# Optimization experiments

Measured on AMD Instinct MI355X. Metric: run time of the kernel, lower is better.

The kernel has to match this reference:

```python
import jax, jax.numpy as jnp
import numpy as np

OFFSET = (0, 0)
STRIDE = (2, 2)

B, C, H, W = 2, 256, 384, 384
N_ACTIVE = 16384
GRID = 192  # strided index grid: OFFSET + (GRID-1)*STRIDE < H


def setup_inputs() -> dict:
    key = jax.random.key(0)
    k1, k2, k3 = jax.random.split(key, 3)
    x = jax.random.normal(k1, (B, C, N_ACTIVE), dtype=jnp.float32)
    original_output = jax.random.normal(k2, (B, C, H, W), dtype=jnp.float32)
    active_indices = jax.random.randint(k3, (N_ACTIVE, 2), 0, GRID, dtype=jnp.int32)
    return {"x": x, "original_output": original_output, "active_indices": active_indices}


def reference(x, original_output, active_indices):
    # Scatter-write active values into the dense output at strided/offset coords.
    # write location for active index k: (OFFSET[0] + iy*STRIDE[0], OFFSET[1] + ix*STRIDE[1])
    h = OFFSET[0] + active_indices[:, 0] * STRIDE[0]  # [N]
    w = OFFSET[1] + active_indices[:, 1] * STRIDE[1]  # [N]
    # advanced indexing on the two spatial dims -> [B, C, N] slots, overwritten by x
    out = original_output.at[:, :, h, w].set(x)
    return out
```

## Files before the change

### kernel.cpp

```cpp
#include <hip/hip_runtime.h>

#define BB      2
#define CC      256
#define HH      384
#define WW      384
#define N_ACT   16384
#define GRID_N  192
#define NCELL   (GRID_N * GRID_N)
#define PLANE_F4 ((HH * WW) / 4)
#define ROW_F4   (WW / 4)
#define PAIRS_PER_PLANE (PLANE_F4 / 2)
#define BLK_PER_PLANE (PAIRS_PER_PLANE / 256)
#define NXCD    8

typedef float fx4 __attribute__((ext_vector_type(4)));

__global__ void winner_scatter_kernel(const int2* __restrict__ idx,
                                      int* __restrict__ winner) {
    int k = blockIdx.x * blockDim.x + threadIdx.x;
    if (k < N_ACT) {
        int2 p = idx[k];
        atomicMax(&winner[p.x * GRID_N + p.y], k);
    }
}

__global__ void scatter_main_kernel(const fx4* __restrict__ orig,
                                    const float* __restrict__ x,
                                    const int* __restrict__ winner,
                                    fx4* __restrict__ out) {
    int L   = blockIdx.x;
    int xcd = L & (NXCD - 1);
    int g   = L >> 3;
    int p   = (g / BLK_PER_PLANE) * NXCD + xcd;
    int j   = g % BLK_PER_PLANE;

    int q   = j * 256 + threadIdx.x;
    int gy  = q / ROW_F4;
    int col = q - gy * ROW_F4;

    int base = p * PLANE_F4 + (gy * 2) * ROW_F4 + col;

    const int2* wrow2 = reinterpret_cast<const int2*>(winner + gy * GRID_N);
    int2 w = wrow2[col];
    fx4 ve = __builtin_nontemporal_load(&orig[base]);
    fx4 vo = __builtin_nontemporal_load(&orig[base + ROW_F4]);

    if (w.x >= 0 || w.y >= 0) {
        const float* xp = x + p * N_ACT;
        if (w.x >= 0) ve[0] = xp[w.x];
        if (w.y >= 0) ve[2] = xp[w.y];
    }

    __builtin_nontemporal_store(ve, &out[base]);
    __builtin_nontemporal_store(vo, &out[base + ROW_F4]);
}

extern "C" void kernel_launch(void* const* d_in, const int* in_sizes, int n_in,
                              void* d_out, int out_size, void* d_ws, size_t ws_size,
                              hipStream_t stream) {
    const float* x    = (const float*)d_in[0];
    const float* orig = (const float*)d_in[1];
    const int*   idx  = (const int*)d_in[2];
    float*       out  = (float*)d_out;
    int*         winner = (int*)d_ws;

    (void)hipMemsetAsync(winner, 0xFF, NCELL * sizeof(int), stream);
    winner_scatter_kernel<<<dim3((N_ACT + 255) / 256), dim3(256), 0, stream>>>(
        (const int2*)idx, winner);
    scatter_main_kernel<<<dim3(BB * CC * BLK_PER_PLANE), dim3(256), 0, stream>>>(
        (const fx4*)orig, x, winner, (fx4*)out);
}
```

Measured before the change: 129.1 us.

## Split odd-row copy into separate kernel from even-row merge

Splits the fused kernel in two. The first copies the odd rows, which never receive scatter writes, and it does not depend on the winner table. The second handles only the even rows, where winner entries are merged with x. The aim is a simple pure-copy kernel that needs no winner lookups. The cost is an extra kernel launch and a serial dependency between the two launches on the same stream.

```diff
diff --git a/kernel.cpp b/kernel.cpp
--- a/kernel.cpp
+++ b/kernel.cpp
@@ -9,8 +9,10 @@
 #define NCELL   (GRID_N * GRID_N)
 #define PLANE_F4 ((HH * WW) / 4)
 #define ROW_F4   (WW / 4)
-#define PAIRS_PER_PLANE (PLANE_F4 / 2)
-#define BLK_PER_PLANE (PAIRS_PER_PLANE / 256)
+#define EVEN_SLOTS 18432
+#define ODD_HALF   9216
+#define B_BLK_PER_PLANE 72
+#define A_BLK_PER_PLANE 36
 #define NXCD    8
 
 typedef float fx4 __attribute__((ext_vector_type(4)));
@@ -24,15 +26,32 @@
     }
 }
 
-__global__ void scatter_main_kernel(const fx4* __restrict__ orig,
-                                    const float* __restrict__ x,
-                                    const int* __restrict__ winner,
-                                    fx4* __restrict__ out) {
+__global__ void copy_odd_kernel(const fx4* __restrict__ orig,
+                                fx4* __restrict__ out) {
+    int L = blockIdx.x;
+    int p = L / A_BLK_PER_PLANE;
+    int j = L - p * A_BLK_PER_PLANE;
+    int s = j * 256 + threadIdx.x;
+    int gy  = s / ROW_F4;
+    int col = s - gy * ROW_F4;
+    int a  = p * PLANE_F4 + (2 * gy + 1) * ROW_F4 + col;
+    int a2 = a + PLANE_F4 / 2;
+
+    fx4 v1 = __builtin_nontemporal_load(&orig[a]);
+    fx4 v2 = __builtin_nontemporal_load(&orig[a2]);
+    __builtin_nontemporal_store(v1, &out[a]);
+    __builtin_nontemporal_store(v2, &out[a2]);
+}
+
+__global__ void merge_even_kernel(const fx4* __restrict__ orig,
+                                  const float* __restrict__ x,
+                                  const int* __restrict__ winner,
+                                  fx4* __restrict__ out) {
     int L   = blockIdx.x;
     int xcd = L & (NXCD - 1);
     int g   = L >> 3;
-    int p   = (g / BLK_PER_PLANE) * NXCD + xcd;
-    int j   = g % BLK_PER_PLANE;
+    int p   = (g / B_BLK_PER_PLANE) * NXCD + xcd;
+    int j   = g % B_BLK_PER_PLANE;
 
     int q   = j * 256 + threadIdx.x;
     int gy  = q / ROW_F4;
@@ -43,7 +62,6 @@
     const int2* wrow2 = reinterpret_cast<const int2*>(winner + gy * GRID_N);
     int2 w = wrow2[col];
     fx4 ve = __builtin_nontemporal_load(&orig[base]);
-    fx4 vo = __builtin_nontemporal_load(&orig[base + ROW_F4]);
 
     if (w.x >= 0 || w.y >= 0) {
         const float* xp = x + p * N_ACT;
@@ -52,7 +70,6 @@
     }
 
     __builtin_nontemporal_store(ve, &out[base]);
-    __builtin_nontemporal_store(vo, &out[base + ROW_F4]);
 }
 
 extern "C" void kernel_launch(void* const* d_in, const int* in_sizes, int n_in,
@@ -67,6 +84,8 @@
     (void)hipMemsetAsync(winner, 0xFF, NCELL * sizeof(int), stream);
     winner_scatter_kernel<<<dim3((N_ACT + 255) / 256), dim3(256), 0, stream>>>(
         (const int2*)idx, winner);
-    scatter_main_kernel<<<dim3(BB * CC * BLK_PER_PLANE), dim3(256), 0, stream>>>(
+    copy_odd_kernel<<<dim3(BB * CC * A_BLK_PER_PLANE), dim3(256), 0, stream>>>(
+        (const fx4*)orig, (fx4*)out);
+    merge_even_kernel<<<dim3(BB * CC * B_BLK_PER_PLANE), dim3(256), 0, stream>>>(
         (const fx4*)orig, x, winner, (fx4*)out);
 }
```

After: 145.3 us. 1.13x slower.
